# Performance work log

Hardware: AMD Instinct MI355X
Metric: run time of the kernel (lower is better)

## Reference

```python
import jax, jax.numpy as jnp
import numpy as np

D_MODEL = 512
N_HEADS = 8
D_K = D_MODEL // N_HEADS
LN_EPS = 1e-5


def setup_inputs() -> dict:
    key = jax.random.key(0)
    ks = jax.random.split(key, 12)
    B, S = 2, 2048
    sc = 1.0 / np.sqrt(D_MODEL)
    inp = {
        'q': jax.random.normal(ks[0], (B, S, D_MODEL), jnp.float32),
        'k': jax.random.normal(ks[1], (B, S, D_MODEL), jnp.float32),
        'v': jax.random.normal(ks[2], (B, S, D_MODEL), jnp.float32),
        'Wq': jax.random.normal(ks[3], (D_MODEL, D_MODEL), jnp.float32) * sc,
        'bq': jnp.zeros((D_MODEL,), jnp.float32),
        'Wk': jax.random.normal(ks[4], (D_MODEL, D_MODEL), jnp.float32) * sc,
        'bk': jnp.zeros((D_MODEL,), jnp.float32),
        'Wv': jax.random.normal(ks[5], (D_MODEL, D_MODEL), jnp.float32) * sc,
        'bv': jnp.zeros((D_MODEL,), jnp.float32),
        'Wo': jax.random.normal(ks[6], (D_MODEL, D_MODEL), jnp.float32) * sc,
        'bo': jnp.zeros((D_MODEL,), jnp.float32),
        'gamma': jnp.ones((D_MODEL,), jnp.float32),
        'beta': jnp.zeros((D_MODEL,), jnp.float32),
    }
    return inp


def _split_heads(x):
    B, S, _ = x.shape
    return x.reshape(B, S, N_HEADS, D_K).transpose(0, 2, 1, 3)  # [B,H,S,d_k]


def reference(q, k, v, Wq, bq, Wk, bk, Wv, bv, Wo, bo, gamma, beta):
    B, S, _ = q.shape
    Q = _split_heads(q @ Wq.T + bq)
    K = _split_heads(k @ Wk.T + bk)
    V = _split_heads(v @ Wv.T + bv)
    scores = jnp.einsum('bhqd,bhkd->bhqk', Q, K) / jnp.sqrt(jnp.float32(D_K))
    attn = jax.nn.softmax(scores, axis=-1)  # [B,H,S,S]
    out = jnp.einsum('bhqk,bhkd->bhqd', attn, V)
    out = out.transpose(0, 2, 1, 3).reshape(B, S, D_MODEL)
    out = out @ Wo.T + bo
    x = out + q  # residual
    mu = jnp.mean(x, axis=-1, keepdims=True)
    var = jnp.mean(jnp.square(x - mu), axis=-1, keepdims=True)
    y = (x - mu) * jax.lax.rsqrt(var + LN_EPS) * gamma + beta
    return (y, attn)
```

## Files before the change

kernel.cpp:

```cpp
#include <hip/hip_runtime.h>
#include <hip/hip_bf16.h>

typedef __attribute__((ext_vector_type(8))) short short8;
typedef __attribute__((ext_vector_type(4))) short short4v;
typedef __attribute__((ext_vector_type(4))) float f32x4;

#define MFMA16(A, B, C) __builtin_amdgcn_mfma_f32_16x16x32_bf16(A, B, C, 0, 0, 0)

#define SEQ 2048
#define DM 512
#define NH 8
#define DK 64
#define NROWS 4096
#define DSPLIT 4
#define ASPLIT 2
#define NT_D (SEQ / DSPLIT / 64)
#define NT_A (SEQ / ASPLIT / 64)
#define C1 0.180336880f

__device__ __forceinline__ short f2bf(float f) {
  union { float f; unsigned u; } x; x.f = f;
  unsigned r = (x.u + 0x7fffu + ((x.u >> 16) & 1u)) >> 16;
  return (short)r;
}
__device__ __forceinline__ float bf2f(short s) {
  union { unsigned u; float f; } x; x.u = ((unsigned)(unsigned short)s) << 16;
  return x.f;
}

__global__ __launch_bounds__(256) void cast3_kernel(
    const float* __restrict__ a, const float* __restrict__ b, const float* __restrict__ c,
    short* __restrict__ ab, short* __restrict__ bb, short* __restrict__ cb)
{
  int z = blockIdx.z;
  const float* src = (z == 0) ? a : (z == 1) ? b : c;
  short* dst = (z == 0) ? ab : (z == 1) ? bb : cb;
  size_t i = ((size_t)blockIdx.x * 256 + threadIdx.x) * 8;
  float4 f0 = *(const float4*)(src + i);
  float4 f1 = *(const float4*)(src + i + 4);
  short8 s;
  s[0] = f2bf(f0.x); s[1] = f2bf(f0.y); s[2] = f2bf(f0.z); s[3] = f2bf(f0.w);
  s[4] = f2bf(f1.x); s[5] = f2bf(f1.y); s[6] = f2bf(f1.z); s[7] = f2bf(f1.w);
  *(short8*)(dst + i) = s;
}

__global__ __launch_bounds__(256) void cast4_kernel(
    const float* __restrict__ a, const float* __restrict__ b,
    const float* __restrict__ c, const float* __restrict__ d,
    short* __restrict__ ab, short* __restrict__ bb,
    short* __restrict__ cb, short* __restrict__ db)
{
  int z = blockIdx.z;
  const float* src = (z == 0) ? a : (z == 1) ? b : (z == 2) ? c : d;
  short* dst = (z == 0) ? ab : (z == 1) ? bb : (z == 2) ? cb : db;
  size_t i = ((size_t)blockIdx.x * 256 + threadIdx.x) * 8;
  float4 f0 = *(const float4*)(src + i);
  float4 f1 = *(const float4*)(src + i + 4);
  short8 s;
  s[0] = f2bf(f0.x); s[1] = f2bf(f0.y); s[2] = f2bf(f0.z); s[3] = f2bf(f0.w);
  s[4] = f2bf(f1.x); s[5] = f2bf(f1.y); s[6] = f2bf(f1.z); s[7] = f2bf(f1.w);
  *(short8*)(dst + i) = s;
}

__global__ __launch_bounds__(256) void qkv_proj_kernel(
    const short* __restrict__ qbf, const short* __restrict__ kbf, const short* __restrict__ vbf,
    const short* __restrict__ Wqb, const short* __restrict__ Wkb, const short* __restrict__ Wvb,
    const float* __restrict__ bq, const float* __restrict__ bk, const float* __restrict__ bv,
    short* __restrict__ Qb, short* __restrict__ Kb, short* __restrict__ Vtb)
{
  int z = blockIdx.z;
  const short* X    = (z == 0) ? qbf : (z == 1) ? kbf : vbf;
  const short* W    = (z == 0) ? Wqb : (z == 1) ? Wkb : Wvb;
  const float* bias = (z == 0) ? bq  : (z == 1) ? bk  : bv;

  __shared__ short As[64][40];
  __shared__ short Bs[64][40];

  int t = threadIdx.x;
  int lane = t & 63, wave = t >> 6;
  int wr = wave >> 1, wc = wave & 1;
  int fr = lane & 15, fg = lane >> 4;
  int m0 = blockIdx.x * 64, n0 = blockIdx.y * 64;
  int lrow = t >> 2, lcol = (t & 3) * 8;

  f32x4 acc[2][2] = {};

  short8 a_pf = *(const short8*)(X + (size_t)(m0 + lrow) * DM + lcol);
  short8 b_pf = *(const short8*)(W + (size_t)(n0 + lrow) * DM + lcol);

  for (int k0 = 0; k0 < DM; k0 += 32) {
    __syncthreads();
    *(short8*)&As[lrow][lcol] = a_pf;
    *(short8*)&Bs[lrow][lcol] = b_pf;
    __syncthreads();
    if (k0 + 32 < DM) {
      a_pf = *(const short8*)(X + (size_t)(m0 + lrow) * DM + k0 + 32 + lcol);
      b_pf = *(const short8*)(W + (size_t)(n0 + lrow) * DM + k0 + 32 + lcol);
    }
    short8 a0 = *(const short8*)&As[wr * 32 + fr][fg * 8];
    short8 a1 = *(const short8*)&As[wr * 32 + 16 + fr][fg * 8];
    short8 b0 = *(const short8*)&Bs[wc * 32 + fr][fg * 8];
    short8 b1 = *(const short8*)&Bs[wc * 32 + 16 + fr][fg * 8];
    acc[0][0] = MFMA16(a0, b0, acc[0][0]);
    acc[0][1] = MFMA16(a0, b1, acc[0][1]);
    acc[1][0] = MFMA16(a1, b0, acc[1][0]);
    acc[1][1] = MFMA16(a1, b1, acc[1][1]);
  }

#pragma unroll
  for (int mi = 0; mi < 2; mi++)
#pragma unroll
    for (int ni = 0; ni < 2; ni++)
#pragma unroll
      for (int r = 0; r < 4; r++) {
        int row = m0 + wr * 32 + mi * 16 + fg * 4 + r;
        int col = n0 + wc * 32 + ni * 16 + fr;
        float val = acc[mi][ni][r] + bias[col];
        int bb = row >> 11, s = row & 2047, h = col >> 6, dk = col & 63;
        short o = f2bf(val);
        if (z == 0)      Qb[((size_t)(bb * NH + h) * SEQ + s) * DK + dk] = o;
        else if (z == 1) Kb[((size_t)(bb * NH + h) * SEQ + s) * DK + dk] = o;
        else             Vtb[((size_t)(bb * NH + h) * DK + dk) * SEQ + s] = o;
      }
}

__global__ __launch_bounds__(256) void den_kernel(
    const short* __restrict__ Q, const short* __restrict__ K, float* __restrict__ dp)
{
  __shared__ short Ks[64][72];

  int t = threadIdx.x, lane = t & 63, wave = t >> 6;
  int fr = lane & 15, fg = lane >> 4;
  int bh = blockIdx.y, z = blockIdx.z;
  const short* Qh = Q + (size_t)bh * SEQ * DK;
  const short* Kh = K + (size_t)bh * SEQ * DK;
  int q0 = blockIdx.x * 64 + wave * 16;
  const int kbase = z * (SEQ / DSPLIT);

  short8 qa0 = *(const short8*)(Qh + (q0 + fr) * DK + fg * 8);
  short8 qa1 = *(const short8*)(Qh + (q0 + fr) * DK + 32 + fg * 8);

  int r_st = t >> 2, c_st = (t & 3) * 16;

  const short* kp0 = Kh + (size_t)(kbase + r_st) * DK + c_st;
  short8 k_pf0 = *(const short8*)kp0;
  short8 k_pf1 = *(const short8*)(kp0 + 8);

  float esum = 0.f;

  for (int kt = 0; kt < NT_D; kt++) {
    __syncthreads();
    *(short8*)&Ks[r_st][c_st]     = k_pf0;
    *(short8*)&Ks[r_st][c_st + 8] = k_pf1;
    __syncthreads();
    if (kt + 1 < NT_D) {
      const short* kp = Kh + (size_t)(kbase + (kt + 1) * 64 + r_st) * DK + c_st;
      k_pf0 = *(const short8*)kp;
      k_pf1 = *(const short8*)(kp + 8);
    }
#pragma unroll
    for (int ct = 0; ct < 4; ct++) {
      short8 k0v = *(const short8*)&Ks[ct * 16 + fr][fg * 8];
      short8 k1v = *(const short8*)&Ks[ct * 16 + fr][32 + fg * 8];
      f32x4 zz = {0.f, 0.f, 0.f, 0.f};
      zz = MFMA16(k0v, qa0, zz);
      zz = MFMA16(k1v, qa1, zz);
#pragma unroll
      for (int r = 0; r < 4; r++)
        esum += __builtin_amdgcn_exp2f(zz[r] * C1);
    }
  }

  esum += __shfl_xor(esum, 16);
  esum += __shfl_xor(esum, 32);
  if (lane < 16)
    dp[((size_t)z * 16 + bh) * SEQ + q0 + lane] = esum;
}

__global__ __launch_bounds__(256) void attn_pv_kernel(
    const short* __restrict__ Q, const short* __restrict__ K, const short* __restrict__ Vt,
    const float* __restrict__ dp, float* __restrict__ attn, short* __restrict__ ctxp)
{
  __shared__ short Ks[64][72];
  __shared__ short Vs[64][72];
  __shared__ short P[4][16][72];

  int t = threadIdx.x, lane = t & 63, wave = t >> 6;
  int fr = lane & 15, fg = lane >> 4;
  int bh = blockIdx.y, z = blockIdx.z;
  const short* Qh = Q + (size_t)bh * SEQ * DK;
  const short* Kh = K + (size_t)bh * SEQ * DK;
  const short* Vh = Vt + (size_t)bh * DK * SEQ;
  int q0 = blockIdx.x * 64 + wave * 16;
  const int kbase = z * (SEQ / ASPLIT);

  short8 qa0 = *(const short8*)(Qh + (q0 + fr) * DK + fg * 8);
  short8 qa1 = *(const short8*)(Qh + (q0 + fr) * DK + 32 + fg * 8);

  float dsum = 0.f;
#pragma unroll
  for (int zz = 0; zz < DSPLIT; zz++)
    dsum += dp[((size_t)zz * 16 + bh) * SEQ + q0 + fr];
  float lg2r = -__builtin_amdgcn_logf(dsum);

  int r_st = t >> 2, c_st = (t & 3) * 16;

  f32x4 oacc[4] = {};

  const short* kp0 = Kh + (size_t)(kbase + r_st) * DK + c_st;
  const short* vp0 = Vh + (size_t)r_st * SEQ + kbase + c_st;
  short8 k_pf0 = *(const short8*)kp0;
  short8 k_pf1 = *(const short8*)(kp0 + 8);
  short8 v_pf0 = *(const short8*)vp0;
  short8 v_pf1 = *(const short8*)(vp0 + 8);

  for (int kt = 0; kt < NT_A; kt++) {
    int kb = kbase + kt * 64;
    __syncthreads();
    *(short8*)&Ks[r_st][c_st]     = k_pf0;
    *(short8*)&Ks[r_st][c_st + 8] = k_pf1;
    *(short8*)&Vs[r_st][c_st]     = v_pf0;
    *(short8*)&Vs[r_st][c_st + 8] = v_pf1;
    __syncthreads();
    if (kt + 1 < NT_A) {
      const short* kp = Kh + (size_t)(kb + 64 + r_st) * DK + c_st;
      const short* vp = Vh + (size_t)r_st * SEQ + kb + 64 + c_st;
      k_pf0 = *(const short8*)kp;
      k_pf1 = *(const short8*)(kp + 8);
      v_pf0 = *(const short8*)vp;
      v_pf1 = *(const short8*)(vp + 8);
    }

#pragma unroll
    for (int ct = 0; ct < 4; ct++) {
      short8 k0v = *(const short8*)&Ks[ct * 16 + fr][fg * 8];
      short8 k1v = *(const short8*)&Ks[ct * 16 + fr][32 + fg * 8];
      f32x4 zz = {0.f, 0.f, 0.f, 0.f};
      zz = MFMA16(k0v, qa0, zz);
      zz = MFMA16(k1v, qa1, zz);
      f32x4 p;
#pragma unroll
      for (int r = 0; r < 4; r++)
        p[r] = __builtin_amdgcn_exp2f(zz[r] * C1 + lg2r);
      __builtin_nontemporal_store(p,
          (f32x4*)&attn[((size_t)(bh * SEQ + q0 + fr)) * SEQ + kb + ct * 16 + fg * 4]);
      short4v pk;
#pragma unroll
      for (int r = 0; r < 4; r++) pk[r] = f2bf(p[r]);
      *(short4v*)&P[wave][fr][ct * 16 + fg * 4] = pk;
    }
    asm volatile("s_waitcnt lgkmcnt(0)" ::: "memory");

    short8 pa0 = *(const short8*)&P[wave][fr][fg * 8];
    short8 pa1 = *(const short8*)&P[wave][fr][32 + fg * 8];
#pragma unroll
    for (int dt = 0; dt < 4; dt++) {
      short8 v0 = *(const short8*)&Vs[dt * 16 + fr][fg * 8];
      short8 v1 = *(const short8*)&Vs[dt * 16 + fr][32 + fg * 8];
      oacc[dt] = MFMA16(pa0, v0, oacc[dt]);
      oacc[dt] = MFMA16(pa1, v1, oacc[dt]);
    }
  }

  int b = bh >> 3, h = bh & 7;
#pragma unroll
  for (int dt = 0; dt < 4; dt++)
#pragma unroll
    for (int r = 0; r < 4; r++) {
      int row = q0 + fg * 4 + r;
      ctxp[((size_t)z * NROWS + (size_t)b * SEQ + row) * DM + h * 64 + dt * 16 + fr] =
          f2bf(oacc[dt][r]);
    }
}

__global__ __launch_bounds__(256) void oproj_kernel(
    const short* __restrict__ ctxp, const short* __restrict__ Wob,
    const float* __restrict__ bias, const float* __restrict__ resid,
    float* __restrict__ xout)
{
  const size_t NPART = (size_t)NROWS * DM;
  __shared__ short As[64][40];
  __shared__ short Bs[64][40];

  int t = threadIdx.x;
  int lane = t & 63, wave = t >> 6;
  int wr = wave >> 1, wc = wave & 1;
  int fr = lane & 15, fg = lane >> 4;
  int m0 = blockIdx.x * 64, n0 = blockIdx.y * 64;
  int lrow = t >> 2, lcol = (t & 3) * 8;

  f32x4 acc[2][2] = {};

  size_t ia0 = (size_t)(m0 + lrow) * DM + lcol;
  short8 a_pf0 = *(const short8*)(ctxp + ia0);
  short8 a_pf1 = *(const short8*)(ctxp + NPART + ia0);
  short8 b_pf = *(const short8*)(Wob + (size_t)(n0 + lrow) * DM + lcol);

  for (int k0 = 0; k0 < DM; k0 += 32) {
    __syncthreads();
    {
      short8 sv;
#pragma unroll
      for (int j = 0; j < 8; j++)
        sv[j] = f2bf(bf2f(a_pf0[j]) + bf2f(a_pf1[j]));
      *(short8*)&As[lrow][lcol] = sv;
      *(short8*)&Bs[lrow][lcol] = b_pf;
    }
    __syncthreads();
    if (k0 + 32 < DM) {
      size_t ia = (size_t)(m0 + lrow) * DM + k0 + 32 + lcol;
      a_pf0 = *(const short8*)(ctxp + ia);
      a_pf1 = *(const short8*)(ctxp + NPART + ia);
      b_pf = *(const short8*)(Wob + (size_t)(n0 + lrow) * DM + k0 + 32 + lcol);
    }
    short8 a0 = *(const short8*)&As[wr * 32 + fr][fg * 8];
    short8 a1 = *(const short8*)&As[wr * 32 + 16 + fr][fg * 8];
    short8 b0 = *(const short8*)&Bs[wc * 32 + fr][fg * 8];
    short8 b1 = *(const short8*)&Bs[wc * 32 + 16 + fr][fg * 8];
    acc[0][0] = MFMA16(a0, b0, acc[0][0]);
    acc[0][1] = MFMA16(a0, b1, acc[0][1]);
    acc[1][0] = MFMA16(a1, b0, acc[1][0]);
    acc[1][1] = MFMA16(a1, b1, acc[1][1]);
  }

#pragma unroll
  for (int mi = 0; mi < 2; mi++)
#pragma unroll
    for (int ni = 0; ni < 2; ni++)
#pragma unroll
      for (int r = 0; r < 4; r++) {
        int row = m0 + wr * 32 + mi * 16 + fg * 4 + r;
        int col = n0 + wc * 32 + ni * 16 + fr;
        float val = acc[mi][ni][r] + bias[col] + resid[(size_t)row * DM + col];
        xout[(size_t)row * DM + col] = val;
      }
}

__global__ __launch_bounds__(256) void ln_kernel(
    const float* __restrict__ x, const float* __restrict__ gamma,
    const float* __restrict__ beta, float* __restrict__ y)
{
  int row = blockIdx.x * 4 + (threadIdx.x >> 6);
  int lane = threadIdx.x & 63;
  const float4* xr = (const float4*)(x + (size_t)row * DM);
  float4 v0 = xr[lane * 2];
  float4 v1 = xr[lane * 2 + 1];
  float s = v0.x + v0.y + v0.z + v0.w + v1.x + v1.y + v1.z + v1.w;
#pragma unroll
  for (int off = 1; off < 64; off <<= 1) s += __shfl_xor(s, off);
  float mean = s * (1.0f / DM);
  float a0 = v0.x - mean, a1 = v0.y - mean, a2 = v0.z - mean, a3 = v0.w - mean;
  float a4 = v1.x - mean, a5 = v1.y - mean, a6 = v1.z - mean, a7 = v1.w - mean;
  float vs = a0 * a0 + a1 * a1 + a2 * a2 + a3 * a3 + a4 * a4 + a5 * a5 + a6 * a6 + a7 * a7;
#pragma unroll
  for (int off = 1; off < 64; off <<= 1) vs += __shfl_xor(vs, off);
  float rstd = rsqrtf(vs * (1.0f / DM) + 1e-5f);
  const float4* gp = (const float4*)gamma;
  const float4* bp = (const float4*)beta;
  float4 g0 = gp[lane * 2], g1 = gp[lane * 2 + 1];
  float4 b0 = bp[lane * 2], b1 = bp[lane * 2 + 1];
  float4 o0, o1;
  o0.x = a0 * rstd * g0.x + b0.x; o0.y = a1 * rstd * g0.y + b0.y;
  o0.z = a2 * rstd * g0.z + b0.z; o0.w = a3 * rstd * g0.w + b0.w;
  o1.x = a4 * rstd * g1.x + b1.x; o1.y = a5 * rstd * g1.y + b1.y;
  o1.z = a6 * rstd * g1.z + b1.z; o1.w = a7 * rstd * g1.w + b1.w;
  float4* yr = (float4*)(y + (size_t)row * DM);
  yr[lane * 2] = o0;
  yr[lane * 2 + 1] = o1;
}

extern "C" void kernel_launch(void* const* d_in, const int* in_sizes, int n_in,
                              void* d_out, int out_size, void* d_ws, size_t ws_size,
                              hipStream_t stream)
{
  const float* q     = (const float*)d_in[0];
  const float* k     = (const float*)d_in[1];
  const float* v     = (const float*)d_in[2];
  const float* Wq    = (const float*)d_in[3];
  const float* bq    = (const float*)d_in[4];
  const float* Wk    = (const float*)d_in[5];
  const float* bk    = (const float*)d_in[6];
  const float* Wv    = (const float*)d_in[7];
  const float* bv    = (const float*)d_in[8];
  const float* Wo    = (const float*)d_in[9];
  const float* bo    = (const float*)d_in[10];
  const float* gamma = (const float*)d_in[11];
  const float* beta  = (const float*)d_in[12];

  char* w = (char*)d_ws;
  short* qbf  = (short*)(w);
  short* kbf  = (short*)(w + ((size_t)4  << 20));
  short* vbf  = (short*)(w + ((size_t)8  << 20));
  short* Qb   = (short*)(w + ((size_t)12 << 20));
  short* Kb   = (short*)(w + ((size_t)16 << 20));
  short* Vtb  = (short*)(w + ((size_t)20 << 20));
  short* Wqb  = (short*)(w + ((size_t)24 << 20));
  short* Wkb  = (short*)(w + ((size_t)24 << 20) + ((size_t)512 << 10));
  short* Wvb  = (short*)(w + ((size_t)25 << 20));
  short* Wob  = (short*)(w + ((size_t)25 << 20) + ((size_t)512 << 10));
  float* denp = (float*)(w + ((size_t)26 << 20));
  short* ctxp = (short*)(w);
  float* xbuf = (float*)(w + ((size_t)8 << 20));

  float* y = (float*)d_out;
  float* attnp = y + (size_t)NROWS * DM;

  cast3_kernel<<<dim3(1024, 1, 3), 256, 0, stream>>>(q, k, v, qbf, kbf, vbf);
  cast4_kernel<<<dim3(128, 1, 4), 256, 0, stream>>>(Wq, Wk, Wv, Wo, Wqb, Wkb, Wvb, Wob);
  qkv_proj_kernel<<<dim3(64, 8, 3), 256, 0, stream>>>(qbf, kbf, vbf, Wqb, Wkb, Wvb,
                                                      bq, bk, bv, Qb, Kb, Vtb);
  den_kernel<<<dim3(32, 16, DSPLIT), 256, 0, stream>>>(Qb, Kb, denp);
  attn_pv_kernel<<<dim3(32, 16, ASPLIT), 256, 0, stream>>>(Qb, Kb, Vtb, denp, attnp, ctxp);
  oproj_kernel<<<dim3(64, 8), 256, 0, stream>>>(ctxp, Wob, bo, q, xbuf);
  ln_kernel<<<1024, 256, 0, stream>>>(xbuf, gamma, beta, y);
}
```

Baseline: 162.7 us.

## Split attention-PV over four key chunks and store attention via LDS transpose

Raises the key-axis split of the attention/PV kernel from 2 to 4, so the grid doubles and each block handles half as many key tiles. The four partial context buffers are summed in the output projection, and one of them moves to a separate workspace region because of space. The score MFMA operands are swapped so each lane holds key columns. Probabilities are staged as bf16 in LDS and read back row-wise for coalesced stores, but this writes bf16-rounded values into the fp32 attention output and uses __expf with a reciprocal instead of exp2 with a log offset. The extra partials add context write and read traffic in exchange for more parallelism.

```diff
diff --git a/kernel.cpp b/kernel.cpp
--- a/kernel.cpp
+++ b/kernel.cpp
@@ -13,7 +13,7 @@
 #define DK 64
 #define NROWS 4096
 #define DSPLIT 4
-#define ASPLIT 2
+#define ASPLIT 4
 #define NT_D (SEQ / DSPLIT / 64)
 #define NT_A (SEQ / ASPLIT / 64)
 #define C1 0.180336880f
@@ -179,7 +179,8 @@
 
 __global__ __launch_bounds__(256) void attn_pv_kernel(
     const short* __restrict__ Q, const short* __restrict__ K, const short* __restrict__ Vt,
-    const float* __restrict__ dp, float* __restrict__ attn, short* __restrict__ ctxp)
+    const float* __restrict__ dp, float* __restrict__ attn,
+    short* __restrict__ ctxp0, short* __restrict__ ctxp3)
 {
   __shared__ short Ks[64][72];
   __shared__ short Vs[64][72];
@@ -197,13 +198,19 @@
   short8 qa0 = *(const short8*)(Qh + (q0 + fr) * DK + fg * 8);
   short8 qa1 = *(const short8*)(Qh + (q0 + fr) * DK + 32 + fg * 8);
 
-  float dsum = 0.f;
-#pragma unroll
-  for (int zz = 0; zz < DSPLIT; zz++)
-    dsum += dp[((size_t)zz * 16 + bh) * SEQ + q0 + fr];
-  float lg2r = -__builtin_amdgcn_logf(dsum);
+  float rden[4];
+#pragma unroll
+  for (int r = 0; r < 4; r++) {
+    int row = q0 + fg * 4 + r;
+    float d = 0.f;
+#pragma unroll
+    for (int zz = 0; zz < DSPLIT; zz++)
+      d += dp[((size_t)zz * 16 + bh) * SEQ + row];
+    rden[r] = 1.f / d;
+  }
 
   int r_st = t >> 2, c_st = (t & 3) * 16;
+  int rlo = lane >> 4, c4 = (lane & 15) * 4;
 
   f32x4 oacc[4] = {};
 
@@ -231,25 +238,34 @@
       v_pf1 = *(const short8*)(vp + 8);
     }
 
+    f32x4 sc[4];
 #pragma unroll
     for (int ct = 0; ct < 4; ct++) {
       short8 k0v = *(const short8*)&Ks[ct * 16 + fr][fg * 8];
       short8 k1v = *(const short8*)&Ks[ct * 16 + fr][32 + fg * 8];
       f32x4 zz = {0.f, 0.f, 0.f, 0.f};
-      zz = MFMA16(k0v, qa0, zz);
-      zz = MFMA16(k1v, qa1, zz);
-      f32x4 p;
-#pragma unroll
-      for (int r = 0; r < 4; r++)
-        p[r] = __builtin_amdgcn_exp2f(zz[r] * C1 + lg2r);
-      __builtin_nontemporal_store(p,
-          (f32x4*)&attn[((size_t)(bh * SEQ + q0 + fr)) * SEQ + kb + ct * 16 + fg * 4]);
-      short4v pk;
-#pragma unroll
-      for (int r = 0; r < 4; r++) pk[r] = f2bf(p[r]);
-      *(short4v*)&P[wave][fr][ct * 16 + fg * 4] = pk;
-    }
+      zz = MFMA16(qa0, k0v, zz);
+      zz = MFMA16(qa1, k1v, zz);
+      sc[ct] = zz;
+    }
+
+#pragma unroll
+    for (int ct = 0; ct < 4; ct++)
+#pragma unroll
+      for (int r = 0; r < 4; r++) {
+        float p = __expf(sc[ct][r] * 0.125f) * rden[r];
+        P[wave][fg * 4 + r][ct * 16 + fr] = f2bf(p);
+      }
     asm volatile("s_waitcnt lgkmcnt(0)" ::: "memory");
+
+#pragma unroll
+    for (int jr = 0; jr < 4; jr++) {
+      int row = jr * 4 + rlo;
+      short4v pv4 = *(const short4v*)&P[wave][row][c4];
+      f32x4 vv = {bf2f(pv4[0]), bf2f(pv4[1]), bf2f(pv4[2]), bf2f(pv4[3])};
+      __builtin_nontemporal_store(vv,
+          (f32x4*)&attn[((size_t)(bh * SEQ + q0 + row)) * SEQ + kb + c4]);
+    }
 
     short8 pa0 = *(const short8*)&P[wave][fr][fg * 8];
     short8 pa1 = *(const short8*)&P[wave][fr][32 + fg * 8];
@@ -263,18 +279,19 @@
   }
 
   int b = bh >> 3, h = bh & 7;
+  short* cbase = (z < 3) ? (ctxp0 + (size_t)z * NROWS * DM) : ctxp3;
 #pragma unroll
   for (int dt = 0; dt < 4; dt++)
 #pragma unroll
     for (int r = 0; r < 4; r++) {
       int row = q0 + fg * 4 + r;
-      ctxp[((size_t)z * NROWS + (size_t)b * SEQ + row) * DM + h * 64 + dt * 16 + fr] =
-          f2bf(oacc[dt][r]);
+      cbase[((size_t)b * SEQ + row) * DM + h * 64 + dt * 16 + fr] = f2bf(oacc[dt][r]);
     }
 }
 
 __global__ __launch_bounds__(256) void oproj_kernel(
-    const short* __restrict__ ctxp, const short* __restrict__ Wob,
+    const short* __restrict__ ctxp0, const short* __restrict__ ctxp3,
+    const short* __restrict__ Wob,
     const float* __restrict__ bias, const float* __restrict__ resid,
     float* __restrict__ xout)
 {
@@ -292,8 +309,10 @@
   f32x4 acc[2][2] = {};
 
   size_t ia0 = (size_t)(m0 + lrow) * DM + lcol;
-  short8 a_pf0 = *(const short8*)(ctxp + ia0);
-  short8 a_pf1 = *(const short8*)(ctxp + NPART + ia0);
+  short8 a_pf0 = *(const short8*)(ctxp0 + ia0);
+  short8 a_pf1 = *(const short8*)(ctxp0 + NPART + ia0);
+  short8 a_pf2 = *(const short8*)(ctxp0 + 2 * NPART + ia0);
+  short8 a_pf3 = *(const short8*)(ctxp3 + ia0);
   short8 b_pf = *(const short8*)(Wob + (size_t)(n0 + lrow) * DM + lcol);
 
   for (int k0 = 0; k0 < DM; k0 += 32) {
@@ -302,15 +321,17 @@
       short8 sv;
 #pragma unroll
       for (int j = 0; j < 8; j++)
-        sv[j] = f2bf(bf2f(a_pf0[j]) + bf2f(a_pf1[j]));
+        sv[j] = f2bf(bf2f(a_pf0[j]) + bf2f(a_pf1[j]) + bf2f(a_pf2[j]) + bf2f(a_pf3[j]));
       *(short8*)&As[lrow][lcol] = sv;
       *(short8*)&Bs[lrow][lcol] = b_pf;
     }
     __syncthreads();
     if (k0 + 32 < DM) {
       size_t ia = (size_t)(m0 + lrow) * DM + k0 + 32 + lcol;
-      a_pf0 = *(const short8*)(ctxp + ia);
-      a_pf1 = *(const short8*)(ctxp + NPART + ia);
+      a_pf0 = *(const short8*)(ctxp0 + ia);
+      a_pf1 = *(const short8*)(ctxp0 + NPART + ia);
+      a_pf2 = *(const short8*)(ctxp0 + 2 * NPART + ia);
+      a_pf3 = *(const short8*)(ctxp3 + ia);
       b_pf = *(const short8*)(Wob + (size_t)(n0 + lrow) * DM + k0 + 32 + lcol);
     }
     short8 a0 = *(const short8*)&As[wr * 32 + fr][fg * 8];
@@ -399,8 +420,9 @@
   short* Wvb  = (short*)(w + ((size_t)25 << 20));
   short* Wob  = (short*)(w + ((size_t)25 << 20) + ((size_t)512 << 10));
   float* denp = (float*)(w + ((size_t)26 << 20));
-  short* ctxp = (short*)(w);
-  float* xbuf = (float*)(w + ((size_t)8 << 20));
+  short* ctxp0 = (short*)(w);
+  short* ctxp3 = (short*)(w + ((size_t)27 << 20));
+  float* xbuf  = (float*)(w + ((size_t)12 << 20));
 
   float* y = (float*)d_out;
   float* attnp = y + (size_t)NROWS * DM;
@@ -410,7 +432,8 @@
   qkv_proj_kernel<<<dim3(64, 8, 3), 256, 0, stream>>>(qbf, kbf, vbf, Wqb, Wkb, Wvb,
                                                       bq, bk, bv, Qb, Kb, Vtb);
   den_kernel<<<dim3(32, 16, DSPLIT), 256, 0, stream>>>(Qb, Kb, denp);
-  attn_pv_kernel<<<dim3(32, 16, ASPLIT), 256, 0, stream>>>(Qb, Kb, Vtb, denp, attnp, ctxp);
-  oproj_kernel<<<dim3(64, 8), 256, 0, stream>>>(ctxp, Wob, bo, q, xbuf);
+  attn_pv_kernel<<<dim3(32, 16, ASPLIT), 256, 0, stream>>>(Qb, Kb, Vtb, denp, attnp,
+                                                           ctxp0, ctxp3);
+  oproj_kernel<<<dim3(64, 8), 256, 0, stream>>>(ctxp0, ctxp3, Wob, bo, q, xbuf);
   ln_kernel<<<1024, 256, 0, stream>>>(xbuf, gamma, beta, y);
 }
```

Measured after the change: 130.2 us. 20.0% less time.
